# Optimization experiments

Hardware: AMD Instinct MI355X
Metric: run time of the kernel (lower is better)

Reference implementation:

```python
import jax, jax.numpy as jnp
import numpy as np

H = 1024        # hidden_size
NH = 16         # num_heads
HD = H // NH    # head_dim
DFF = 4 * H
SCALE = HD ** -0.5
EPS = 1e-5


def _ln(x, g, b):
    m = jnp.mean(x, axis=-1, keepdims=True)
    v = jnp.var(x, axis=-1, keepdims=True)
    return (x - m) * jax.lax.rsqrt(v + EPS) * g + b


def _heads(t, B):
    # [B, S, H] -> [B, NH, S, HD]
    return t.reshape(B, -1, NH, HD).transpose(0, 2, 1, 3)


def _merge(t, B):
    # [B, NH, S, HD] -> [B, S, H]
    return t.transpose(0, 2, 1, 3).reshape(B, -1, H)


def _attn(q, k, v):
    s = jnp.einsum('bhqd,bhkd->bhqk', q, k) * SCALE
    p = jax.nn.softmax(s, axis=-1)
    p = jnp.nan_to_num(p, nan=0.0)
    return jnp.einsum('bhqk,bhkd->bhqd', p, v)


def setup_inputs() -> dict:
    key = jax.random.key(0)
    ks = jax.random.split(key, 16)
    std = (2.0 / (5 * H)) ** 0.5
    B, S, SI = 2, 2048, 256
    d = {
        'x': jax.random.normal(ks[0], (B, S, H), jnp.float32),
        'image_features': jax.random.normal(ks[1], (B, SI, H), jnp.float32),
    }
    names = ['sq', 'sk', 'sv', 'so', 'cq', 'ck', 'cv', 'co']
    for i, n in enumerate(names):
        d['W_' + n] = std * jax.random.normal(ks[2 + i], (H, H), jnp.float32)
        d['b_' + n] = jnp.zeros((H,), jnp.float32)
    d['W_ff1'] = std * jax.random.normal(ks[10], (H, DFF), jnp.float32)
    d['b_ff1'] = jnp.zeros((DFF,), jnp.float32)
    d['W_ff2'] = std * jax.random.normal(ks[11], (DFF, H), jnp.float32)
    d['b_ff2'] = jnp.zeros((H,), jnp.float32)
    for n in ['ln1', 'ln2', 'ln3']:
        d['g_' + n] = jnp.ones((H,), jnp.float32)
        d['b_' + n] = jnp.zeros((H,), jnp.float32)
    return d


def reference(x, image_features,
              W_sq, b_sq, W_sk, b_sk, W_sv, b_sv, W_so, b_so,
              W_cq, b_cq, W_ck, b_ck, W_cv, b_cv, W_co, b_co,
              W_ff1, b_ff1, W_ff2, b_ff2,
              g_ln1, b_ln1, g_ln2, b_ln2, g_ln3, b_ln3):
    B = x.shape[0]
    x = x * 0.1
    img = image_features * 0.1

    # --- self attention (pre-norm) ---
    nx = _ln(x, g_ln1, b_ln1)
    q = _heads(nx @ W_sq + b_sq, B)
    k = _heads(nx @ W_sk + b_sk, B)
    v = _heads(nx @ W_sv + b_sv, B)
    so = _merge(_attn(q, k, v), B) @ W_so + b_so
    x = x + so

    # --- cross attention (pre-norm) ---
    nx = _ln(x, g_ln2, b_ln2)
    q = _heads(nx @ W_cq + b_cq, B)
    k = _heads(img @ W_ck + b_ck, B)
    v = _heads(img @ W_cv + b_cv, B)
    co = _merge(_attn(q, k, v), B) @ W_co + b_co
    x = x + co

    # --- feed forward (pre-norm) ---
    nx = _ln(x, g_ln3, b_ln3)
    ff = jax.nn.gelu(nx @ W_ff1 + b_ff1, approximate=False) @ W_ff2 + b_ff2
    x = x + ff
    return x * 10.0
```

## Files before the change

### kernel.cpp

```cpp
#include <hip/hip_runtime.h>
#include <hip/hip_bf16.h>

typedef __bf16 bf16;
typedef __bf16 bf16x4 __attribute__((ext_vector_type(4)));
typedef __bf16 bf16x8 __attribute__((ext_vector_type(8)));
typedef float  f32x4  __attribute__((ext_vector_type(4)));
typedef float  f32x16 __attribute__((ext_vector_type(16)));
typedef int    int4v  __attribute__((ext_vector_type(4)));

#define H_DIM 1024
#define NHEAD 16
#define HD    64
#define QSCL 0.18033688011112042f

__device__ __forceinline__ void gload_lds16(const bf16* g, bf16* l) {
    __builtin_amdgcn_global_load_lds((const __attribute__((address_space(1))) void*)g,
                                     (__attribute__((address_space(3))) void*)l, 16, 0, 0);
}

__device__ __forceinline__ unsigned cvtpk_bf16(float lo, float hi) {
    unsigned r;
    asm volatile("v_cvt_pk_bf16_f32 %0, %1, %2" : "=v"(r) : "v"(lo), "v"(hi));
    return r;
}

__device__ __forceinline__ float fexp2(float x) {
    float r;
    asm("v_exp_f32 %0, %1" : "=v"(r) : "v"(x));
    return r;
}

__device__ __forceinline__ void wconv_body(const float* __restrict__ W,
                                           bf16* __restrict__ Wt, int K, int N,
                                           int bx, int by, int t) {
    __shared__ float tile[64][65];
    const int n0 = bx * 64, k0 = by * 64;
#pragma unroll
    for (int p = 0; p < 4; ++p) {
        int lin = p * 1024 + t * 4;
        int r = lin >> 6, c = lin & 63;
        f32x4 v = *(const f32x4*)(W + (size_t)(k0 + r) * N + n0 + c);
        tile[r][c]     = v[0];
        tile[r][c + 1] = v[1];
        tile[r][c + 2] = v[2];
        tile[r][c + 3] = v[3];
    }
    __syncthreads();
#pragma unroll
    for (int p = 0; p < 4; ++p) {
        int lin = p * 1024 + t * 4;
        int rn = lin >> 6, ck = lin & 63;
        bf16x4 o;
#pragma unroll
        for (int j = 0; j < 4; ++j) o[j] = (bf16)tile[ck + j][rn];
        *(bf16x4*)(Wt + (size_t)(n0 + rn) * K + k0 + ck) = o;
    }
}

__global__ __launch_bounds__(256) void wconv_kernel(const float* __restrict__ W,
                                                    bf16* __restrict__ Wt,
                                                    int K, int N) {
    wconv_body(W, Wt, K, N, blockIdx.x, blockIdx.y, threadIdx.x);
}

struct WPtrs { const float* w[8]; bf16* o[8]; };
__global__ __launch_bounds__(256) void wconv8_kernel(WPtrs p) {
    const int m = blockIdx.z;
    wconv_body(p.w[m], p.o[m], 1024, 1024, blockIdx.x, blockIdx.y, threadIdx.x);
}

__global__ __launch_bounds__(256) void ln_kernel(const float* __restrict__ in, float inScale,
                                                 const float* __restrict__ g,
                                                 const float* __restrict__ b,
                                                 bf16* __restrict__ out) {
    const int row = blockIdx.x, t = threadIdx.x;
    const float* p = in + (size_t)row * H_DIM;
    f32x4 v = *(const f32x4*)(p + t * 4);
    v *= inScale;
    float s1 = v[0] + v[1] + v[2] + v[3];
    float s2 = v[0] * v[0] + v[1] * v[1] + v[2] * v[2] + v[3] * v[3];
#pragma unroll
    for (int m = 1; m < 64; m <<= 1) {
        s1 += __shfl_xor(s1, m);
        s2 += __shfl_xor(s2, m);
    }
    __shared__ float red[8];
    const int wave = t >> 6;
    if ((t & 63) == 0) { red[wave * 2] = s1; red[wave * 2 + 1] = s2; }
    __syncthreads();
    s1 = red[0] + red[2] + red[4] + red[6];
    s2 = red[1] + red[3] + red[5] + red[7];
    float mean = s1 * (1.0f / H_DIM);
    float var  = s2 * (1.0f / H_DIM) - mean * mean;
    float inv  = rsqrtf(var + 1e-5f);
    f32x4 gg = *(const f32x4*)(g + t * 4);
    f32x4 bb = *(const f32x4*)(b + t * 4);
    bf16x4 o;
#pragma unroll
    for (int j = 0; j < 4; ++j) o[j] = (bf16)((v[j] - mean) * inv * gg[j] + bb[j]);
    *(bf16x4*)(out + (size_t)row * H_DIM + t * 4) = o;
}

__global__ __launch_bounds__(256) void cvt_scale_kernel(const float* __restrict__ in,
                                                        bf16* __restrict__ out,
                                                        float s, int n4) {
    int i = blockIdx.x * 256 + threadIdx.x;
    if (i < n4) {
        f32x4 v = *(const f32x4*)(in + (size_t)i * 4);
        bf16x4 o;
#pragma unroll
        for (int j = 0; j < 4; ++j) o[j] = (bf16)(v[j] * s);
        *(bf16x4*)(out + (size_t)i * 4) = o;
    }
}

template <int BM, int BN, int MODE, bool OUT_BF16, bool GELU_EPI, bool HAS_RES>
__global__ __launch_bounds__(256) void gemm_kernel(const bf16* __restrict__ A,
                                                   const bf16* __restrict__ Bt,
                                                   const float* __restrict__ bias1,
                                                   const float* __restrict__ bias2,
                                                   const float* __restrict__ bias3,
                                                   const float* __restrict__ res,
                                                   void* __restrict__ o1, void* __restrict__ o2,
                                                   void* __restrict__ o3,
                                                   int M, int N, int K,
                                                   float resScale, float outScale, int slog2) {
    constexpr int CHUNKS = (BM + BN) / 32;
    constexpr int WRR = BM / 2, WCC = BN / 2;
    constexpr int MI = WRR / 32, NJ = WCC / 32;
    __shared__ bf16 SM[2][(BM + BN) * 64];
    const int nwg = gridDim.x * gridDim.y;
    const int dlin = blockIdx.y * gridDim.x + blockIdx.x;
    const int id = (dlin & 7) * (nwg >> 3) + (dlin >> 3);
    const int bx = id % gridDim.x, by = id / gridDim.x;
    const int m0 = by * BM, n0 = bx * BN;
    const int tid = threadIdx.x;
    const int wave = tid >> 6, lane = tid & 63;
    const int l31 = lane & 31, l5 = lane >> 5;
    const int wr = wave >> 1, wc = wave & 1;
    const int sr = lane >> 3, sc8 = (lane & 7) * 8;
    const int sc8x = sc8 ^ (sr << 3);
    const int rxr = (l31 & 7) << 3;

    f32x16 acc[MI][NJ] = {};

    auto stage = [&](int buf, int k0) {
#pragma unroll
        for (int p = 0; p < CHUNKS; ++p) {
            const int rr = p * 32 + wave * 8 + sr;
            bf16* l = &SM[buf][0] + p * 2048 + wave * 512;
            const bf16* g = (p < BM / 32)
                ? (A  + (size_t)(m0 + rr) * K + k0 + sc8x)
                : (Bt + (size_t)(n0 + rr - BM) * K + k0 + sc8x);
            gload_lds16(g, l);
        }
    };

    stage(0, 0);
    int buf = 0;
    for (int k0 = 0; k0 < K; k0 += 64) {
        const bool pre = (k0 + 64 < K);
        if (pre) {
            stage(buf ^ 1, k0 + 64);
            asm volatile("s_waitcnt vmcnt(%0)" :: "i"(CHUNKS) : "memory");
        } else {
            asm volatile("s_waitcnt vmcnt(0)" ::: "memory");
        }
        __builtin_amdgcn_sched_barrier(0);
        __builtin_amdgcn_s_barrier();
#pragma unroll
        for (int kk = 0; kk < 4; ++kk) {
            const int sa = (kk * 16 + l5 * 8) ^ rxr;
            bf16x8 af[MI], bfr[NJ];
#pragma unroll
            for (int i = 0; i < MI; ++i)
                af[i] = *(const bf16x8*)&SM[buf][(wr * WRR + i * 32 + l31) * 64 + sa];
#pragma unroll
            for (int j = 0; j < NJ; ++j)
                bfr[j] = *(const bf16x8*)&SM[buf][(BM + wc * WCC + j * 32 + l31) * 64 + sa];
#pragma unroll
            for (int i = 0; i < MI; ++i)
#pragma unroll
                for (int j = 0; j < NJ; ++j)
                    acc[i][j] = __builtin_amdgcn_mfma_f32_32x32x16_bf16(af[i], bfr[j], acc[i][j], 0, 0, 0);
        }
        __builtin_amdgcn_s_barrier();
        buf ^= 1;
    }

#pragma unroll
    for (int i = 0; i < MI; ++i) {
#pragma unroll
        for (int j = 0; j < NJ; ++j) {
            const int col = n0 + wc * WCC + j * 32 + l31;
            const int rbase = m0 + wr * WRR + i * 32 + l5 * 4;
            if (MODE == 0) {
                const float bv = bias1[col];
#pragma unroll
                for (int rq = 0; rq < 4; ++rq)
#pragma unroll
                    for (int rr = 0; rr < 4; ++rr) {
                        const int row = rbase + rq * 8 + rr;
                        const size_t idx = (size_t)row * N + col;
                        float v = acc[i][j][rq * 4 + rr] + bv;
                        if (HAS_RES) v += res[idx] * resScale;
                        if (GELU_EPI) v = 0.5f * v * (1.0f + erff(v * 0.70710678118654752f));
                        v *= outScale;
                        if (OUT_BF16) ((bf16*)o1)[idx] = (bf16)v;
                        else          ((float*)o1)[idx] = v;
                    }
            } else {
                const int sec = col >> 10, cl = col & 1023;
                const bool isV = (MODE == 1) ? (sec == 2) : (sec == 1);
                const float* bp = (MODE == 1) ? (sec == 0 ? bias1 : sec == 1 ? bias2 : bias3)
                                              : (sec == 0 ? bias1 : bias2);
                const float bv = bp[cl];
                if (!isV) {
                    bf16* dst = (MODE == 1) ? (sec == 0 ? (bf16*)o1 : (bf16*)o2) : (bf16*)o1;
                    const float sc = (MODE == 1 && sec == 0) ? outScale : 1.f;
#pragma unroll
                    for (int rq = 0; rq < 4; ++rq)
#pragma unroll
                        for (int rr = 0; rr < 4; ++rr) {
                            const int row = rbase + rq * 8 + rr;
                            dst[(size_t)row * H_DIM + cl] = (bf16)((acc[i][j][rq * 4 + rr] + bv) * sc);
                        }
                } else {
                    bf16* dst = (MODE == 1) ? (bf16*)o3 : (bf16*)o2;
                    const int S = 1 << slog2;
                    const int hI = cl >> 6, dI = cl & 63;
#pragma unroll
                    for (int rq = 0; rq < 4; ++rq) {
                        const int row0 = rbase + rq * 8;
                        const int bI = row0 >> slog2, s0 = row0 & (S - 1);
                        bf16x4 ov;
#pragma unroll
                        for (int rr = 0; rr < 4; ++rr) ov[rr] = (bf16)(acc[i][j][rq * 4 + rr] + bv);
                        *(bf16x4*)(dst + ((size_t)((bI * NHEAD + hI) * HD + dI)) * S + s0) = ov;
                    }
                }
            }
        }
    }
}

__global__ __launch_bounds__(256) void attn_kernel(const bf16* __restrict__ Qb,
                                                   const bf16* __restrict__ Kb,
                                                   const bf16* __restrict__ Vt_g,
                                                   bf16* __restrict__ Ob,
                                                   int SQ, int SK) {
    __shared__ bf16 SMEM[2][2][64 * 64];
    const int nwg = gridDim.x * gridDim.y;
    const int dlin = blockIdx.y * gridDim.x + blockIdx.x;
    const int id = (dlin & 7) * (nwg >> 3) + (dlin >> 3);
    const int NQ = gridDim.y;
    const int bh = id / NQ, qt = id - bh * NQ;
    const int b = bh >> 4, h = bh & 15;
    const int q0 = qt * 128;
    const int tid = threadIdx.x, wave = tid >> 6, lane = tid & 63;
    const int lr = lane & 15, lhi = lane >> 4;

    bf16x8 qf[2][2];
#pragma unroll
    for (int qi = 0; qi < 2; ++qi) {
        const bf16* qp = Qb + ((size_t)b * SQ + q0 + wave * 32 + qi * 16 + lr) * H_DIM + h * HD;
        qf[qi][0] = *(const bf16x8*)(qp + lhi * 8);
        qf[qi][1] = *(const bf16x8*)(qp + 32 + lhi * 8);
    }

    const int kx = (((lr & 3) | (((lr >> 2) & 1) << 2)) << 3);
    const int vx = (((lr & 3) | (((lr >> 3) & 1) << 2)) << 3);
    int krow[4];
#pragma unroll
    for (int nf = 0; nf < 4; ++nf)
        krow[nf] = (nf >> 1) * 32 + (lr >> 2) * 8 + (nf & 1) * 4 + (lr & 3);

    const int rS = tid >> 3, cS = (tid & 7) * 8;
    const int kxw = (((rS & 3) | (((rS >> 3) & 1) << 2)) << 3);
    const bf16* Kg = Kb + (size_t)b * SK * H_DIM + h * HD;
    const bf16* Vg = Vt_g + (size_t)bh * 64 * SK;

    bf16x8 onesv;
#pragma unroll
    for (int j = 0; j < 8; ++j) onesv[j] = (bf16)1.0f;

    f32x4 o[2][4] = {};
    f32x4 psum[2] = {};
    bf16x8 gK[2], gV[2];

    auto LOADG = [&](int kb) {
#pragma unroll
        for (int p = 0; p < 2; ++p) {
            gK[p] = *(const bf16x8*)(Kg + (size_t)(kb + p * 32 + rS) * H_DIM + cS);
            gV[p] = *(const bf16x8*)(Vg + (size_t)(p * 32 + rS) * SK + kb + cS);
        }
    };
    auto STORES = [&](int buf) {
#pragma unroll
        for (int p = 0; p < 2; ++p) {
            *(bf16x8*)&SMEM[buf][0][(p * 32 + rS) * 64 + (cS ^ kxw)] = gK[p];
            *(bf16x8*)&SMEM[buf][1][(p * 32 + rS) * 64 + (cS ^ kxw)] = gV[p];
        }
    };
    auto COMPUTE = [&](int buf) {
        f32x4 s[2][4] = {};
        __builtin_amdgcn_s_setprio(1);
#pragma unroll
        for (int nf = 0; nf < 4; ++nf) {
            const int base = krow[nf] * 64;
            bf16x8 kf0 = *(const bf16x8*)&SMEM[buf][0][base + ((lhi * 8) ^ kx)];
            bf16x8 kf1 = *(const bf16x8*)&SMEM[buf][0][base + ((32 + lhi * 8) ^ kx)];
#pragma unroll
            for (int qi = 0; qi < 2; ++qi) {
                s[qi][nf] = __builtin_amdgcn_mfma_f32_16x16x32_bf16(kf0, qf[qi][0], s[qi][nf], 0, 0, 0);
                s[qi][nf] = __builtin_amdgcn_mfma_f32_16x16x32_bf16(kf1, qf[qi][1], s[qi][nf], 0, 0, 0);
            }
        }
        __builtin_amdgcn_s_setprio(0);
        unsigned pw[2][8];
#pragma unroll
        for (int qi = 0; qi < 2; ++qi)
#pragma unroll
            for (int nf = 0; nf < 4; ++nf) {
                float p0 = fexp2(s[qi][nf][0]);
                float p1 = fexp2(s[qi][nf][1]);
                float p2 = fexp2(s[qi][nf][2]);
                float p3 = fexp2(s[qi][nf][3]);
                pw[qi][nf * 2]     = cvtpk_bf16(p0, p1);
                pw[qi][nf * 2 + 1] = cvtpk_bf16(p2, p3);
            }
        __builtin_amdgcn_s_setprio(1);
#pragma unroll
        for (int kk = 0; kk < 2; ++kk) {
            bf16x8 pb[2];
#pragma unroll
            for (int qi = 0; qi < 2; ++qi) {
                int4v w = { (int)pw[qi][kk * 4], (int)pw[qi][kk * 4 + 1],
                            (int)pw[qi][kk * 4 + 2], (int)pw[qi][kk * 4 + 3] };
                pb[qi] = __builtin_bit_cast(bf16x8, w);
                psum[qi] = __builtin_amdgcn_mfma_f32_16x16x32_bf16(onesv, pb[qi], psum[qi], 0, 0, 0);
            }
#pragma unroll
            for (int df = 0; df < 4; ++df) {
                bf16x8 vf = *(const bf16x8*)&SMEM[buf][1][(df * 16 + lr) * 64 + ((kk * 32 + lhi * 8) ^ vx)];
                o[0][df] = __builtin_amdgcn_mfma_f32_16x16x32_bf16(vf, pb[0], o[0][df], 0, 0, 0);
                o[1][df] = __builtin_amdgcn_mfma_f32_16x16x32_bf16(vf, pb[1], o[1][df], 0, 0, 0);
            }
        }
        __builtin_amdgcn_s_setprio(0);
    };

    const int nt = SK >> 6;
    LOADG(0);
    STORES(0);
    if (nt > 1) LOADG(64);
    __syncthreads();
    for (int t = 0; t < nt; ++t) {
        COMPUTE(t & 1);
        if (t + 1 < nt) {
            STORES((t + 1) & 1);
            if (t + 2 < nt) LOADG((t + 2) << 6);
        }
        __syncthreads();
    }

    bf16* T = &SMEM[0][0][0] + wave * (32 * 72);
#pragma unroll
    for (int qi = 0; qi < 2; ++qi) {
        const float inv = 1.0f / psum[qi][0];
#pragma unroll
        for (int df = 0; df < 4; ++df)
#pragma unroll
            for (int r = 0; r < 4; ++r)
                T[(qi * 16 + lr) * 72 + df * 16 + lhi * 4 + r] = (bf16)(o[qi][df][r] * inv);
    }
#pragma unroll
    for (int pp = 0; pp < 4; ++pp) {
        const int r32 = pp * 8 + (lane >> 3), ch = (lane & 7) * 8;
        bf16x8 v = *(const bf16x8*)&T[r32 * 72 + ch];
        *(bf16x8*)(Ob + ((size_t)b * SQ + q0 + wave * 32 + r32) * H_DIM + h * HD + ch) = v;
    }
}

extern "C" void kernel_launch(void* const* d_in, const int* in_sizes, int n_in,
                              void* d_out, int out_size, void* d_ws, size_t ws_size,
                              hipStream_t stream) {
    const float* x    = (const float*)d_in[0];
    const float* img  = (const float*)d_in[1];
    const float* W_sq = (const float*)d_in[2];   const float* b_sq = (const float*)d_in[3];
    const float* W_sk = (const float*)d_in[4];   const float* b_sk = (const float*)d_in[5];
    const float* W_sv = (const float*)d_in[6];   const float* b_sv = (const float*)d_in[7];
    const float* W_so = (const float*)d_in[8];   const float* b_so = (const float*)d_in[9];
    const float* W_cq = (const float*)d_in[10];  const float* b_cq = (const float*)d_in[11];
    const float* W_ck = (const float*)d_in[12];  const float* b_ck = (const float*)d_in[13];
    const float* W_cv = (const float*)d_in[14];  const float* b_cv = (const float*)d_in[15];
    const float* W_co = (const float*)d_in[16];  const float* b_co = (const float*)d_in[17];
    const float* W_f1 = (const float*)d_in[18];  const float* b_f1 = (const float*)d_in[19];
    const float* W_f2 = (const float*)d_in[20];  const float* b_f2 = (const float*)d_in[21];
    const float* g1 = (const float*)d_in[22];    const float* bb1 = (const float*)d_in[23];
    const float* g2 = (const float*)d_in[24];    const float* bb2 = (const float*)d_in[25];
    const float* g3 = (const float*)d_in[26];    const float* bb3 = (const float*)d_in[27];

    char* ws = (char*)d_ws;
    const size_t MB = 1ull << 20;
    bf16* WT   = (bf16*)ws;
    bf16* w_sq = WT + 0 * (1u << 20);
    bf16* w_sk = WT + 1 * (1u << 20);
    bf16* w_sv = WT + 2 * (1u << 20);
    bf16* w_so = WT + 3 * (1u << 20);
    bf16* w_cq = WT + 4 * (1u << 20);
    bf16* w_ck = WT + 5 * (1u << 20);
    bf16* w_cv = WT + 6 * (1u << 20);
    bf16* w_co = WT + 7 * (1u << 20);
    bf16* w_f1 = WT + 8 * (1u << 20);
    bf16* w_f2 = WT + 12 * (1u << 20);
    float* XR  = (float*)(ws + 32 * MB);
    bf16* NX   = (bf16*)(ws + 48 * MB);
    bf16* Qb   = (bf16*)(ws + 56 * MB);
    bf16* Kb   = (bf16*)(ws + 64 * MB);
    bf16* Vt   = (bf16*)(ws + 72 * MB);
    bf16* FF   = (bf16*)(ws + 56 * MB);
    bf16* IMGB = (bf16*)(ws + 88 * MB);

    const dim3 blk(256);

    WPtrs wp;
    wp.w[0] = W_sq; wp.o[0] = w_sq;  wp.w[1] = W_sk; wp.o[1] = w_sk;
    wp.w[2] = W_sv; wp.o[2] = w_sv;  wp.w[3] = W_so; wp.o[3] = w_so;
    wp.w[4] = W_cq; wp.o[4] = w_cq;  wp.w[5] = W_ck; wp.o[5] = w_ck;
    wp.w[6] = W_cv; wp.o[6] = w_cv;  wp.w[7] = W_co; wp.o[7] = w_co;
    wconv8_kernel<<<dim3(16, 16, 8), blk, 0, stream>>>(wp);
    wconv_kernel<<<dim3(64, 16), blk, 0, stream>>>(W_f1, w_f1, 1024, 4096);
    wconv_kernel<<<dim3(16, 64), blk, 0, stream>>>(W_f2, w_f2, 4096, 1024);

    ln_kernel<<<4096, blk, 0, stream>>>(x, 0.1f, g1, bb1, NX);
    gemm_kernel<128, 128, 1, true, false, false><<<dim3(24, 32), blk, 0, stream>>>(
        NX, w_sq, b_sq, b_sk, b_sv, nullptr, Qb, Kb, Vt, 4096, 3072, 1024, 0.f, QSCL, 11);
    attn_kernel<<<dim3(32, 16), blk, 0, stream>>>(Qb, Kb, Vt, NX, 2048, 2048);
    gemm_kernel<64, 128, 0, false, false, true><<<dim3(8, 64), blk, 0, stream>>>(
        NX, w_so, b_so, nullptr, nullptr, x, XR, nullptr, nullptr, 4096, 1024, 1024, 0.1f, 1.f, 0);

    ln_kernel<<<4096, blk, 0, stream>>>(XR, 1.f, g2, bb2, NX);
    gemm_kernel<64, 128, 0, true, false, false><<<dim3(8, 64), blk, 0, stream>>>(
        NX, w_cq, b_cq, nullptr, nullptr, nullptr, Qb, nullptr, nullptr, 4096, 1024, 1024, 0.f, QSCL, 0);
    cvt_scale_kernel<<<dim3(512), blk, 0, stream>>>(img, IMGB, 0.1f, 131072);
    gemm_kernel<64, 128, 2, true, false, false><<<dim3(16, 8), blk, 0, stream>>>(
        IMGB, w_ck, b_ck, b_cv, nullptr, nullptr, Kb, Vt, nullptr, 512, 2048, 1024, 0.f, 1.f, 8);
    attn_kernel<<<dim3(32, 16), blk, 0, stream>>>(Qb, Kb, Vt, NX, 2048, 256);
    gemm_kernel<64, 128, 0, false, false, true><<<dim3(8, 64), blk, 0, stream>>>(
        NX, w_co, b_co, nullptr, nullptr, XR, XR, nullptr, nullptr, 4096, 1024, 1024, 1.f, 1.f, 0);

    ln_kernel<<<4096, blk, 0, stream>>>(XR, 1.f, g3, bb3, NX);
    gemm_kernel<128, 128, 0, true, true, false><<<dim3(32, 32), blk, 0, stream>>>(
        NX, w_f1, b_f1, nullptr, nullptr, nullptr, FF, nullptr, nullptr, 4096, 4096, 1024, 0.f, 1.f, 0);
    gemm_kernel<64, 128, 0, false, false, true><<<dim3(8, 64), blk, 0, stream>>>(
        FF, w_f2, b_f2, nullptr, nullptr, XR, d_out, nullptr, nullptr, 4096, 1024, 4096, 1.f, 10.f, 0);
}
```

Measured before the change: 284.7 us.

## Run self-attention QKV projection in FP8 with fp8 layernorm output and weights

Adds an FP8 path for the fused QKV projection. Layernorm now writes fp8 activations, a new kernel transposes and converts the three self-attention weights to fp8, and a dedicated GEMM uses 32x32x16 fp8 MFMA with fp8 LDS staging. The aim is to halve operand bytes and use the higher fp8 matrix throughput, at the cost of unscaled fp8 quantization error in Q/K/V and an extra weight-conversion launch. The generic MODE 1 epilogue is removed from the bf16 GEMM.

```diff
diff --git a/kernel.cpp b/kernel.cpp
--- a/kernel.cpp
+++ b/kernel.cpp
@@ -17,11 +17,23 @@
     __builtin_amdgcn_global_load_lds((const __attribute__((address_space(1))) void*)g,
                                      (__attribute__((address_space(3))) void*)l, 16, 0, 0);
 }
+__device__ __forceinline__ void gload_lds16_u8(const unsigned char* g, unsigned char* l) {
+    __builtin_amdgcn_global_load_lds((const __attribute__((address_space(1))) void*)g,
+                                     (__attribute__((address_space(3))) void*)l, 16, 0, 0);
+}
 
 __device__ __forceinline__ unsigned cvtpk_bf16(float lo, float hi) {
     unsigned r;
     asm volatile("v_cvt_pk_bf16_f32 %0, %1, %2" : "=v"(r) : "v"(lo), "v"(hi));
     return r;
+}
+__device__ __forceinline__ unsigned cvt2_fp8(float a, float b) {
+    unsigned r;
+    asm volatile("v_cvt_pk_fp8_f32 %0, %1, %2" : "=v"(r) : "v"(a), "v"(b));
+    return r & 0xffffu;
+}
+__device__ __forceinline__ unsigned pack4_fp8(float a, float b, float c, float d) {
+    return cvt2_fp8(a, b) | (cvt2_fp8(c, d) << 16);
 }
 
 __device__ __forceinline__ float fexp2(float x) {
@@ -67,6 +79,33 @@
 __global__ __launch_bounds__(256) void wconv8_kernel(WPtrs p) {
     const int m = blockIdx.z;
     wconv_body(p.w[m], p.o[m], 1024, 1024, blockIdx.x, blockIdx.y, threadIdx.x);
+}
+
+struct W3Ptrs { const float* w[3]; };
+__global__ __launch_bounds__(256) void wconv_fp8_kernel(W3Ptrs p, unsigned char* __restrict__ out) {
+    __shared__ float tile[64][65];
+    const int m = blockIdx.z, t = threadIdx.x;
+    const float* W = p.w[m];
+    unsigned char* Wt = out + (size_t)m * 1024 * 1024;
+    const int n0 = blockIdx.x * 64, k0 = blockIdx.y * 64;
+#pragma unroll
+    for (int pp = 0; pp < 4; ++pp) {
+        int lin = pp * 1024 + t * 4;
+        int r = lin >> 6, c = lin & 63;
+        f32x4 v = *(const f32x4*)(W + (size_t)(k0 + r) * 1024 + n0 + c);
+        tile[r][c]     = v[0];
+        tile[r][c + 1] = v[1];
+        tile[r][c + 2] = v[2];
+        tile[r][c + 3] = v[3];
+    }
+    __syncthreads();
+#pragma unroll
+    for (int pp = 0; pp < 4; ++pp) {
+        int lin = pp * 1024 + t * 4;
+        int rn = lin >> 6, ck = lin & 63;
+        unsigned u = pack4_fp8(tile[ck][rn], tile[ck + 1][rn], tile[ck + 2][rn], tile[ck + 3][rn]);
+        *(unsigned*)&Wt[(size_t)(n0 + rn) * 1024 + k0 + ck] = u;
+    }
 }
 
 __global__ __launch_bounds__(256) void ln_kernel(const float* __restrict__ in, float inScale,
@@ -99,6 +138,39 @@
 #pragma unroll
     for (int j = 0; j < 4; ++j) o[j] = (bf16)((v[j] - mean) * inv * gg[j] + bb[j]);
     *(bf16x4*)(out + (size_t)row * H_DIM + t * 4) = o;
+}
+
+__global__ __launch_bounds__(256) void ln_fp8_kernel(const float* __restrict__ in, float inScale,
+                                                     const float* __restrict__ g,
+                                                     const float* __restrict__ b,
+                                                     unsigned* __restrict__ out) {
+    const int row = blockIdx.x, t = threadIdx.x;
+    const float* p = in + (size_t)row * H_DIM;
+    f32x4 v = *(const f32x4*)(p + t * 4);
+    v *= inScale;
+    float s1 = v[0] + v[1] + v[2] + v[3];
+    float s2 = v[0] * v[0] + v[1] * v[1] + v[2] * v[2] + v[3] * v[3];
+#pragma unroll
+    for (int m = 1; m < 64; m <<= 1) {
+        s1 += __shfl_xor(s1, m);
+        s2 += __shfl_xor(s2, m);
+    }
+    __shared__ float red[8];
+    const int wave = t >> 6;
+    if ((t & 63) == 0) { red[wave * 2] = s1; red[wave * 2 + 1] = s2; }
+    __syncthreads();
+    s1 = red[0] + red[2] + red[4] + red[6];
+    s2 = red[1] + red[3] + red[5] + red[7];
+    float mean = s1 * (1.0f / H_DIM);
+    float var  = s2 * (1.0f / H_DIM) - mean * mean;
+    float inv  = rsqrtf(var + 1e-5f);
+    f32x4 gg = *(const f32x4*)(g + t * 4);
+    f32x4 bb = *(const f32x4*)(b + t * 4);
+    float y0 = (v[0] - mean) * inv * gg[0] + bb[0];
+    float y1 = (v[1] - mean) * inv * gg[1] + bb[1];
+    float y2 = (v[2] - mean) * inv * gg[2] + bb[2];
+    float y3 = (v[3] - mean) * inv * gg[3] + bb[3];
+    out[row * 256 + t] = pack4_fp8(y0, y1, y2, y3);
 }
 
 __global__ __launch_bounds__(256) void cvt_scale_kernel(const float* __restrict__ in,
@@ -211,22 +283,19 @@
                     }
             } else {
                 const int sec = col >> 10, cl = col & 1023;
-                const bool isV = (MODE == 1) ? (sec == 2) : (sec == 1);
-                const float* bp = (MODE == 1) ? (sec == 0 ? bias1 : sec == 1 ? bias2 : bias3)
-                                              : (sec == 0 ? bias1 : bias2);
-                const float bv = bp[cl];
+                const bool isV = (sec == 1);
+                const float bv = (sec == 0 ? bias1 : bias2)[cl];
                 if (!isV) {
-                    bf16* dst = (MODE == 1) ? (sec == 0 ? (bf16*)o1 : (bf16*)o2) : (bf16*)o1;
-                    const float sc = (MODE == 1 && sec == 0) ? outScale : 1.f;
+                    bf16* dst = (bf16*)o1;
 #pragma unroll
                     for (int rq = 0; rq < 4; ++rq)
 #pragma unroll
                         for (int rr = 0; rr < 4; ++rr) {
                             const int row = rbase + rq * 8 + rr;
-                            dst[(size_t)row * H_DIM + cl] = (bf16)((acc[i][j][rq * 4 + rr] + bv) * sc);
+                            dst[(size_t)row * H_DIM + cl] = (bf16)(acc[i][j][rq * 4 + rr] + bv);
                         }
                 } else {
-                    bf16* dst = (MODE == 1) ? (bf16*)o3 : (bf16*)o2;
+                    bf16* dst = (bf16*)o2;
                     const int S = 1 << slog2;
                     const int hI = cl >> 6, dI = cl & 63;
 #pragma unroll
@@ -238,6 +307,108 @@
                         for (int rr = 0; rr < 4; ++rr) ov[rr] = (bf16)(acc[i][j][rq * 4 + rr] + bv);
                         *(bf16x4*)(dst + ((size_t)((bI * NHEAD + hI) * HD + dI)) * S + s0) = ov;
                     }
+                }
+            }
+        }
+    }
+}
+
+__global__ __launch_bounds__(256) void gemm_qkv_fp8(const unsigned char* __restrict__ A8,
+                                                    const unsigned char* __restrict__ B8,
+                                                    const float* __restrict__ bias1,
+                                                    const float* __restrict__ bias2,
+                                                    const float* __restrict__ bias3,
+                                                    bf16* __restrict__ Qo, bf16* __restrict__ Ko,
+                                                    bf16* __restrict__ Vo) {
+    constexpr int Kd = 1024;
+    __shared__ unsigned char SM[2][256 * 64];
+    const int nwg = gridDim.x * gridDim.y;
+    const int dlin = blockIdx.y * gridDim.x + blockIdx.x;
+    const int id = (dlin & 7) * (nwg >> 3) + (dlin >> 3);
+    const int bx = id % gridDim.x, by = id / gridDim.x;
+    const int m0 = by * 128, n0 = bx * 128;
+    const int tid = threadIdx.x;
+    const int wave = tid >> 6, lane = tid & 63;
+    const int l31 = lane & 31, l5 = lane >> 5;
+    const int wr = wave >> 1, wc = wave & 1;
+    const int srow = wave * 16 + (lane >> 2);
+    const int sunit = (((lane & 3) ^ ((srow >> 1) & 3)) << 4);
+    const int rxc = (l31 >> 1) & 3;
+
+    f32x16 acc[2][2] = {};
+
+    auto stage = [&](int buf, int k0) {
+#pragma unroll
+        for (int p = 0; p < 4; ++p) {
+            const int rr = p * 64 + srow;
+            unsigned char* l = &SM[buf][0] + p * 4096 + wave * 1024;
+            const unsigned char* g = (p < 2)
+                ? (A8 + (size_t)(m0 + rr) * Kd + k0 + sunit)
+                : (B8 + (size_t)(n0 + rr - 128) * Kd + k0 + sunit);
+            gload_lds16_u8(g, l);
+        }
+    };
+
+    stage(0, 0);
+    int buf = 0;
+    for (int k0 = 0; k0 < Kd; k0 += 64) {
+        const bool pre = (k0 + 64 < Kd);
+        if (pre) {
+            stage(buf ^ 1, k0 + 64);
+            asm volatile("s_waitcnt vmcnt(4)" ::: "memory");
+        } else {
+            asm volatile("s_waitcnt vmcnt(0)" ::: "memory");
+        }
+        __builtin_amdgcn_sched_barrier(0);
+        __builtin_amdgcn_s_barrier();
+#pragma unroll
+        for (int kk = 0; kk < 4; ++kk) {
+            const int sa = (((kk ^ rxc) << 4) + l5 * 8);
+            long long af[2], bfr[2];
+#pragma unroll
+            for (int i = 0; i < 2; ++i)
+                af[i] = *(const long long*)&SM[buf][(wr * 64 + i * 32 + l31) * 64 + sa];
+#pragma unroll
+            for (int j = 0; j < 2; ++j)
+                bfr[j] = *(const long long*)&SM[buf][(128 + wc * 64 + j * 32 + l31) * 64 + sa];
+#pragma unroll
+            for (int i = 0; i < 2; ++i)
+#pragma unroll
+                for (int j = 0; j < 2; ++j)
+                    acc[i][j] = __builtin_amdgcn_mfma_f32_32x32x16_fp8_fp8(af[i], bfr[j], acc[i][j], 0, 0, 0);
+        }
+        __builtin_amdgcn_s_barrier();
+        buf ^= 1;
+    }
+
+#pragma unroll
+    for (int i = 0; i < 2; ++i) {
+#pragma unroll
+        for (int j = 0; j < 2; ++j) {
+            const int col = n0 + wc * 64 + j * 32 + l31;
+            const int rbase = m0 + wr * 64 + i * 32 + l5 * 4;
+            const int sec = col >> 10, cl = col & 1023;
+            const float bv = (sec == 0 ? bias1 : sec == 1 ? bias2 : bias3)[cl];
+            if (sec < 2) {
+                bf16* dst = (sec == 0) ? Qo : Ko;
+                const float sc = (sec == 0) ? QSCL : 1.f;
+#pragma unroll
+                for (int rq = 0; rq < 4; ++rq)
+#pragma unroll
+                    for (int rr = 0; rr < 4; ++rr) {
+                        const int row = rbase + rq * 8 + rr;
+                        dst[(size_t)row * H_DIM + cl] = (bf16)((acc[i][j][rq * 4 + rr] + bv) * sc);
+                    }
+            } else {
+                const int hI = cl >> 6, dI = cl & 63;
+#pragma unroll
+                for (int rq = 0; rq < 4; ++rq) {
+                    const int row0 = rbase + rq * 8;
+                    const int bI = row0 >> 11, s0 = row0 & 2047;
+                    bf16x4 ov;
+#pragma unroll
+                    for (int rr = 0; rr < 4; ++rr) ov[rr] = (bf16)(acc[i][j][rq * 4 + rr] + bv);
+                    *(bf16x4*)(Vo + ((size_t)((bI * NHEAD + hI) * HD + dI)) * 2048 + s0) = ov;
                 }
             }
         }
@@ -420,6 +591,8 @@
     bf16* Kb   = (bf16*)(ws + 64 * MB);
     bf16* Vt   = (bf16*)(ws + 72 * MB);
     bf16* FF   = (bf16*)(ws + 56 * MB);
+    unsigned char* W8  = (unsigned char*)(ws + 80 * MB);
+    unsigned char* NX8 = (unsigned char*)(ws + 83 * MB);
     bf16* IMGB = (bf16*)(ws + 88 * MB);
 
     const dim3 blk(256);
@@ -430,12 +603,13 @@
     wp.w[4] = W_cq; wp.o[4] = w_cq;  wp.w[5] = W_ck; wp.o[5] = w_ck;
     wp.w[6] = W_cv; wp.o[6] = w_cv;  wp.w[7] = W_co; wp.o[7] = w_co;
     wconv8_kernel<<<dim3(16, 16, 8), blk, 0, stream>>>(wp);
+    W3Ptrs w3; w3.w[0] = W_sq; w3.w[1] = W_sk; w3.w[2] = W_sv;
+    wconv_fp8_kernel<<<dim3(16, 16, 3), blk, 0, stream>>>(w3, W8);
     wconv_kernel<<<dim3(64, 16), blk, 0, stream>>>(W_f1, w_f1, 1024, 4096);
     wconv_kernel<<<dim3(16, 64), blk, 0, stream>>>(W_f2, w_f2, 4096, 1024);
 
-    ln_kernel<<<4096, blk, 0, stream>>>(x, 0.1f, g1, bb1, NX);
-    gemm_kernel<128, 128, 1, true, false, false><<<dim3(24, 32), blk, 0, stream>>>(
-        NX, w_sq, b_sq, b_sk, b_sv, nullptr, Qb, Kb, Vt, 4096, 3072, 1024, 0.f, QSCL, 11);
+    ln_fp8_kernel<<<4096, blk, 0, stream>>>(x, 0.1f, g1, bb1, (unsigned*)NX8);
+    gemm_qkv_fp8<<<dim3(24, 32), blk, 0, stream>>>(NX8, W8, b_sq, b_sk, b_sv, Qb, Kb, Vt);
     attn_kernel<<<dim3(32, 16), blk, 0, stream>>>(Qb, Kb, Vt, NX, 2048, 2048);
     gemm_kernel<64, 128, 0, false, false, true><<<dim3(8, 64), blk, 0, stream>>>(
         NX, w_so, b_so, nullptr, nullptr, x, XR, nullptr, nullptr, 4096, 1024, 1024, 0.1f, 1.f, 0);
```

Result: faster. 273.5 us (-3.9%).
